# Kernel optimization log

Measured on AMD Instinct MI355X. Metric: run time of the kernel, lower is better.

Reference implementation:

```python
import jax, jax.numpy as jnp
import numpy as np

NUM_HEADS = 16
EMBED_DIM = 1024
HEAD_DIM = EMBED_DIM // NUM_HEADS


def _rel_shift(r):
    # r: (B, tlen, rlen). Pad with ONES (faithful to original), shift, tril.
    B, tlen, rlen = r.shape
    pad = jnp.ones((B, tlen, 1), dtype=r.dtype)
    rp = jnp.concatenate([pad, r], axis=2).reshape(B, rlen + 1, tlen)
    return jnp.tril(rp[:, 1:, :].reshape(B, tlen, rlen))


def setup_inputs() -> dict:
    key = jax.random.key(0)
    ks = jax.random.split(key, 12)
    T, B, E, H, D = 128, 8, EMBED_DIM, NUM_HEADS, HEAD_DIM
    query = jax.random.normal(ks[0], (T, B, E), dtype=jnp.float32)
    key_t = jax.random.normal(ks[1], (T, B, E), dtype=jnp.float32)
    value = jax.random.normal(ks[2], (T, B, E), dtype=jnp.float32)
    rel_pe = jax.random.normal(ks[3], (T, B, E), dtype=jnp.float32)
    # causal mask: True = masked (future positions)
    causal = ~jnp.tril(jnp.ones((T, T), dtype=bool))
    attn_mask = jnp.broadcast_to(causal, (B * H, T, T))
    utt_mask = jnp.ones((B * H, T, T, 1), dtype=jnp.float32)
    spk_mask = jax.random.randint(ks[4], (B, T, T), 0, 2, dtype=jnp.int32)
    s = 1.0 / np.sqrt(E)
    q_w = jax.random.uniform(ks[5], (E, E), jnp.float32, -s, s)
    k_w = jax.random.uniform(ks[6], (E, E), jnp.float32, -s, s)
    v_w = jax.random.uniform(ks[7], (E, E), jnp.float32, -s, s)
    r_w = jax.random.uniform(ks[8], (E, E), jnp.float32, -s, s)
    spk_emb = jax.random.uniform(ks[9], (2, E), jnp.float32, -s, s)
    out_w = jax.random.uniform(ks[10], (E, E), jnp.float32, -s, s)
    return {"query": query, "key": key_t, "value": value, "rel_pe": rel_pe,
            "attn_mask": attn_mask, "utt_mask": utt_mask, "spk_mask": spk_mask,
            "q_w": q_w, "k_w": k_w, "v_w": v_w, "r_w": r_w,
            "spk_emb": spk_emb, "out_w": out_w}


def reference(query, key, value, rel_pe, attn_mask, utt_mask, spk_mask,
              q_w, k_w, v_w, r_w, spk_emb, out_w):
    T, B, E = query.shape
    H, D = NUM_HEADS, HEAD_DIM
    scaling = float(D) ** -0.5

    def split_heads(x):  # (T, B, E) -> (B*H, T, D)
        return x.reshape(T, B * H, D).transpose(1, 0, 2)

    # NOTE: original computes k and v from `query` (faithful)
    q = split_heads(query @ q_w.T)
    k = split_heads(query @ k_w.T)
    v = split_heads(query @ v_w.T)
    r = split_heads(rel_pe @ r_w.T)

    # s_q: speaker embedding row 0 broadcast to all positions
    s_q = split_heads(jnp.broadcast_to(spk_emb[0], (T, B, E)))
    # s_k: (B, T, T, E) -> (B*H, T, T, D), same reshape chain as original
    s_k = spk_emb[spk_mask]                                   # (B, T, T, E)
    s_k = s_k.reshape(B, T * T, E).transpose(1, 0, 2)         # (T*T, B, E)
    s_k = s_k.reshape(T * T, B * H, D).transpose(1, 0, 2)     # (B*H, T*T, D)
    s_k = s_k.reshape(B * H, T, T, D) * utt_mask              # (B*H, T, T, D)

    new_q = q + s_q
    a1 = jnp.einsum('nid,njd->nij', new_q, k)
    a2 = jnp.einsum('nid,nijd->nij', new_q, s_k)
    a3 = _rel_shift(jnp.einsum('nid,njd->nij', s_q, r))

    w = (a1 + a2 + a3) * scaling
    w = jnp.where(attn_mask, jnp.asarray(1e-30, w.dtype), w)
    w = jax.nn.softmax(w, axis=-1)

    out = jnp.einsum('nij,njd->nid', w, v)                    # (B*H, T, D)
    out = out.transpose(1, 0, 2).reshape(T, B, E) @ out_w.T
    return out
```

## Files before the change

### kernel.cpp

```cpp
#include <hip/hip_runtime.h>
#include <hip/hip_bf16.h>
#include <cstddef>
#include <cstdint>


typedef _Float16 f16;
typedef __attribute__((ext_vector_type(8))) _Float16 f16x8;
typedef __attribute__((ext_vector_type(4))) float f32x4;

#define GLOBAL_TO_LDS(g, l) __builtin_amdgcn_global_load_lds( \
    (const __attribute__((address_space(1))) void*)(g),       \
    (__attribute__((address_space(3))) void*)(l), 16, 0, 0)

#define PIPE_SYNC(N) do {                                      \
    asm volatile("s_waitcnt vmcnt(" #N ")" ::: "memory");      \
    __builtin_amdgcn_s_barrier();                              \
    __builtin_amdgcn_sched_barrier(0);                         \
} while (0)

struct Ptr7 { const float* s[7]; };

__global__ __launch_bounds__(256) void tof16_kernel(Ptr7 p, f16* dbase)
{
    const float* s = p.s[blockIdx.y];
    f16* d = dbase + (size_t)blockIdx.y * (1u << 20);
    const int i = (blockIdx.x * 256 + threadIdx.x) * 8;
    const float4 a = *(const float4*)(s + i);
    const float4 b = *(const float4*)(s + i + 4);
    f16x8 o;
    o[0] = (f16)a.x; o[1] = (f16)a.y; o[2] = (f16)a.z; o[3] = (f16)a.w;
    o[4] = (f16)b.x; o[5] = (f16)b.y; o[6] = (f16)b.z; o[7] = (f16)b.w;
    *(f16x8*)(d + i) = o;
}

template <int TM, int TN, class Epi>
__device__ __forceinline__ void gemm3ph(const f16* __restrict__ A,
                                        const f16* __restrict__ B,
                                        int m0, int n0, Epi epi)
{
    constexpr int AITS = TM / 32, BITS = TN / 32;
    constexpr int LD = AITS + BITS;
    constexpr int FM = TM / 32, FN = TN / 32;
    __shared__ __attribute__((aligned(16))) f16 As0[TM * 64];
    __shared__ __attribute__((aligned(16))) f16 As1[TM * 64];
    __shared__ __attribute__((aligned(16))) f16 As2[TM * 64];
    __shared__ __attribute__((aligned(16))) f16 Bs0[TN * 64];
    __shared__ __attribute__((aligned(16))) f16 Bs1[TN * 64];
    __shared__ __attribute__((aligned(16))) f16 Bs2[TN * 64];
    const int tid = threadIdx.x;
    const int wave = tid >> 6, lane = tid & 63;
    const int wr = wave >> 1, wc = wave & 1;
    const int l16 = lane & 15, lk = lane >> 4;
    f32x4 acc[FM][FN] = {};

    auto stage = [&](f16* as_, f16* bs_, int k0) {
#pragma unroll
        for (int it = 0; it < AITS; ++it) {
            const int ebase = it * 2048 + wave * 512;
            const int e = ebase + lane * 8;
            const int row = e >> 6, slot = (e >> 3) & 7;
            const int scol = (slot ^ (row & 7)) << 3;
            GLOBAL_TO_LDS(A + (size_t)(m0 + row) * 1024 + k0 + scol, as_ + ebase);
        }
#pragma unroll
        for (int it = 0; it < BITS; ++it) {
            const int ebase = it * 2048 + wave * 512;
            const int e = ebase + lane * 8;
            const int row = e >> 6, slot = (e >> 3) & 7;
            const int scol = (slot ^ (row & 7)) << 3;
            GLOBAL_TO_LDS(B + (size_t)(n0 + row) * 1024 + k0 + scol, bs_ + ebase);
        }
    };
    auto compute = [&](const f16* as_, const f16* bs_) {
#pragma unroll
        for (int ksl = 0; ksl < 2; ++ksl) {
            const int s = ksl * 4 + lk;
            f16x8 af[FM], bg[FN];
#pragma unroll
            for (int mi = 0; mi < FM; ++mi) {
                const int r = wr * (TM / 2) + mi * 16 + l16;
                af[mi] = *(const f16x8*)(as_ + r * 64 + ((s ^ (r & 7)) << 3));
            }
#pragma unroll
            for (int ni = 0; ni < FN; ++ni) {
                const int r = wc * (TN / 2) + ni * 16 + l16;
                bg[ni] = *(const f16x8*)(bs_ + r * 64 + ((s ^ (r & 7)) << 3));
            }
#pragma unroll
            for (int mi = 0; mi < FM; ++mi)
#pragma unroll
                for (int ni = 0; ni < FN; ++ni)
                    acc[mi][ni] = __builtin_amdgcn_mfma_f32_16x16x32_f16(
                        af[mi], bg[ni], acc[mi][ni], 0, 0, 0);
        }
    };
    auto sync_steady = [&]() {
        if constexpr (LD == 8) PIPE_SYNC(8);
        else if constexpr (LD == 6) PIPE_SYNC(6);
        else PIPE_SYNC(5);
    };

    stage(As0, Bs0, 0);
    stage(As1, Bs1, 64);
    int k = 0;
#pragma unroll 1
    for (int t = 0; t < 15; t += 3) {
        sync_steady();
        if (t + 2 < 16) stage(As2, Bs2, k + 128);
        compute(As0, Bs0);
        sync_steady();
        if (t + 3 < 16) stage(As0, Bs0, k + 192);
        compute(As1, Bs1);
        sync_steady();
        if (t + 4 < 16) stage(As1, Bs1, k + 256);
        compute(As2, Bs2);
        k += 192;
    }
    PIPE_SYNC(0);
    compute(As0, Bs0);

#pragma unroll
    for (int mi = 0; mi < FM; ++mi)
#pragma unroll
        for (int ni = 0; ni < FN; ++ni)
#pragma unroll
            for (int r = 0; r < 4; ++r)
                epi(m0 + wr * (TM / 2) + mi * 16 + lk * 4 + r,
                    n0 + wc * (TN / 2) + ni * 16 + l16, acc[mi][ni][r]);
}

struct EpiHead {
    f16* dst; const float* addvec;
    __device__ void operator()(int row, int col, float v) const {
        const float x = addvec ? v + addvec[col] : v;
        const int b = row & 7, t = row >> 3, h = col >> 6, d = col & 63;
        dst[(size_t)(((b << 4) + h) * 128 + t) * 64 + d] = (f16)x;
    }
};
struct EpiF32 {
    float* dst;
    __device__ void operator()(int row, int col, float v) const {
        dst[(size_t)row * 1024 + col] = v;
    }
};

__global__ __launch_bounds__(256) void proj4_kernel(
    const f16* __restrict__ qf, const f16* __restrict__ rf,
    const f16* __restrict__ wbase, const float* __restrict__ spk_emb,
    f16* __restrict__ Qh, f16* __restrict__ Kh,
    f16* __restrict__ Vh, f16* __restrict__ Rh)
{
    const int bid = blockIdx.x;
    const int z = (bid & 7) >> 1;
    const int w = ((bid >> 3) << 1) | (bid & 1);
    const int m0 = (w >> 3) << 7;
    const int n0 = (w & 7) << 7;
    const f16* A = (z == 3) ? rf : qf;
    const f16* W = wbase + ((size_t)z << 20);
    f16* dst = (z == 0) ? Qh : (z == 1) ? Kh : (z == 2) ? Vh : Rh;
    EpiHead epi{dst, (z == 0) ? spk_emb : nullptr};
    gemm3ph<128, 128>(A, W, m0, n0, epi);
}

__global__ __launch_bounds__(256) void out_kernel(
    const f16* __restrict__ ATT, const f16* __restrict__ owf,
    float* __restrict__ out)
{
    const int bid = blockIdx.x;
    const int m0 = (bid >> 3) << 5;
    const int n0 = (bid & 7) << 7;
    EpiF32 epi{out};
    gemm3ph<32, 128>(ATT, owf, m0, n0, epi);
}

__global__ __launch_bounds__(256) void attn_mfma_kernel(
    const f16* __restrict__ Qh, const f16* __restrict__ Kh,
    const f16* __restrict__ Vh, const f16* __restrict__ Rh,
    const float* __restrict__ spk_emb, const int* __restrict__ spk_mask,
    const float* __restrict__ utt_mask, f16* __restrict__ ATT)
{
    __shared__ __attribute__((aligned(16))) char smem[58880];
    f16* nq = (f16*)smem;
    f16* kt = (f16*)(smem + 8192);
    f16* vt = (f16*)(smem + 24576);
    f16* vs = (f16*)(smem + 40960);
    float* cbuf = (float*)(smem + 57344);
    float* dd   = (float*)(smem + 57856);
    float* sq   = (float*)(smem + 58368);

    const int bx = blockIdx.x, n = bx >> 1, half = bx & 1;
    const int b = n >> 4, h = n & 15, i0 = half << 6;
    const int tid = threadIdx.x, wave = tid >> 6, lane = tid & 63;
    const int l16 = lane & 15, lk = lane >> 4;
    const int il0 = wave * 16 + lk * 4;
    const size_t hb = (size_t)n * (128 * 64);

    if (tid < 128)
        sq[tid] = spk_emb[(tid >> 6) * 1024 + (h << 6) + (tid & 63)];

#pragma unroll
    for (int it = 0; it < 2; ++it) {
        const int ebase = it * 2048 + wave * 512;
        const int e = ebase + lane * 8;
        const int row = e >> 6, slot = (e >> 3) & 7;
        const int scol = (slot ^ (row & 7)) << 3;
        GLOBAL_TO_LDS(Qh + hb + (size_t)(i0 + row) * 64 + scol, nq + ebase);
    }
#pragma unroll
    for (int it = 0; it < 4; ++it) {
        const int ebase = it * 2048 + wave * 512;
        const int e = ebase + lane * 8;
        const int row = e >> 6, slot = (e >> 3) & 7;
        const int scol = (slot ^ (row & 7)) << 3;
        GLOBAL_TO_LDS(Kh + hb + (size_t)row * 64 + scol, kt + ebase);
        GLOBAL_TO_LDS(Vh + hb + (size_t)row * 64 + scol, vs + ebase);
    }

    float du[8][4];
    int   sm[8][4];
#pragma unroll
    for (int ni = 0; ni < 8; ++ni) {
        const int j = ni * 16 + l16;
#pragma unroll
        for (int r = 0; r < 4; ++r) {
            const int i = i0 + il0 + r;
            du[ni][r] = utt_mask[((size_t)n * 128 + i) * 128 + j];
            sm[ni][r] = spk_mask[((size_t)b * 128 + i) * 128 + j];
        }
    }
    __syncthreads();

    {
        const int st = tid >> 1, hf = tid & 1;
        const int jt = st & 15, dt = st >> 4;
        f16x8 v[8];
#pragma unroll
        for (int jj = 0; jj < 8; ++jj) {
            const int j = jt * 8 + jj;
            v[jj] = *(const f16x8*)(vs + j * 64 + ((dt ^ (j & 7)) << 3));
        }
#pragma unroll
        for (int dr = 0; dr < 4; ++dr) {
            f16x8 w;
            int d;
            if (hf == 0) {
                d = dt * 8 + dr;
#pragma unroll
                for (int jj = 0; jj < 8; ++jj) w[jj] = v[jj][dr];
            } else {
                d = dt * 8 + 4 + dr;
#pragma unroll
                for (int jj = 0; jj < 8; ++jj) w[jj] = v[jj][4 + dr];
            }
            *(f16x8*)(vt + d * 128 + ((jt ^ (d & 7)) << 3)) = w;
        }
    }

    if (tid < 128) {
        const int j = tid;
        float s = 0.f;
#pragma unroll
        for (int c = 0; c < 8; ++c) {
            const f16x8 rv = *(const f16x8*)(Rh + hb + (size_t)j * 64 + c * 8);
#pragma unroll
            for (int e = 0; e < 8; ++e)
                s = fmaf((float)rv[e], sq[c * 8 + e], s);
        }
        cbuf[j] = s;
    } else if (tid < 192) {
        const int i = tid - 128;
        float s0 = 0.f, s1 = 0.f;
#pragma unroll
        for (int c = 0; c < 8; ++c) {
            const f16x8 qv = *(const f16x8*)(nq + i * 64 + ((c ^ (i & 7)) << 3));
#pragma unroll
            for (int e = 0; e < 8; ++e) {
                const float q = (float)qv[e];
                s0 = fmaf(q, sq[c * 8 + e], s0);
                s1 = fmaf(q, sq[64 + c * 8 + e], s1);
            }
        }
        dd[i] = s0; dd[64 + i] = s1;
    }
    __syncthreads();

    const int iw = wave * 16 + l16;
    f16x8 af[2];
#pragma unroll
    for (int ksl = 0; ksl < 2; ++ksl) {
        const int s = ksl * 4 + lk;
        af[ksl] = *(const f16x8*)(nq + iw * 64 + ((s ^ (iw & 7)) << 3));
    }
    f32x4 sacc[8] = {};
#pragma unroll
    for (int ksl = 0; ksl < 2; ++ksl) {
        const int s = ksl * 4 + lk;
#pragma unroll
        for (int ni = 0; ni < 8; ++ni) {
            const int j = ni * 16 + l16;
            const f16x8 bg = *(const f16x8*)(kt + j * 64 + ((s ^ (j & 7)) << 3));
            sacc[ni] = __builtin_amdgcn_mfma_f32_16x16x32_f16(af[ksl], bg, sacc[ni], 0, 0, 0);
        }
    }

    float sc[8][4];
#pragma unroll
    for (int ni = 0; ni < 8; ++ni) {
        const int j = ni * 16 + l16;
#pragma unroll
        for (int r = 0; r < 4; ++r) {
            const int il = il0 + r, i = i0 + il;
            const float a2 = du[ni][r] * (sm[ni][r] ? dd[64 + il] : dd[il]);
            const float a3 = (j <= i) ? cbuf[127 - i + j] : 0.f;
            const float v = (sacc[ni][r] + a2 + a3) * 0.125f;
            sc[ni][r] = (j > i) ? 1e-30f : v;
        }
    }
    float inv[4];
    f16* ps = vs + wave * 2048;
#pragma unroll
    for (int r = 0; r < 4; ++r) {
        float m = sc[0][r];
#pragma unroll
        for (int ni = 1; ni < 8; ++ni) m = fmaxf(m, sc[ni][r]);
#pragma unroll
        for (int off = 8; off > 0; off >>= 1) m = fmaxf(m, __shfl_xor(m, off, 64));
        float ssum = 0.f;
#pragma unroll
        for (int ni = 0; ni < 8; ++ni) {
            const float e = __expf(sc[ni][r] - m);
            sc[ni][r] = e;
            ssum += e;
        }
#pragma unroll
        for (int off = 8; off > 0; off >>= 1) ssum += __shfl_xor(ssum, off, 64);
        inv[r] = 1.f / ssum;
    }
#pragma unroll
    for (int ni = 0; ni < 8; ++ni) {
        const int j = ni * 16 + l16;
#pragma unroll
        for (int r = 0; r < 4; ++r) {
            const int il = lk * 4 + r;
            ps[il * 128 + ((((j >> 3) ^ (il & 7)) << 3) | (j & 7))] = (f16)sc[ni][r];
        }
    }

    f16x8 pa[4];
#pragma unroll
    for (int ks = 0; ks < 4; ++ks) {
        const int slot = ks * 4 + lk;
        pa[ks] = *(const f16x8*)(ps + l16 * 128 + ((slot ^ (l16 & 7)) << 3));
    }
    f32x4 oacc[4] = {};
#pragma unroll
    for (int ks = 0; ks < 4; ++ks) {
        const int slot = ks * 4 + lk;
#pragma unroll
        for (int nd = 0; nd < 4; ++nd) {
            const int d = nd * 16 + l16;
            const f16x8 vb = *(const f16x8*)(vt + d * 128 + ((slot ^ (d & 7)) << 3));
            oacc[nd] = __builtin_amdgcn_mfma_f32_16x16x32_f16(pa[ks], vb, oacc[nd], 0, 0, 0);
        }
    }
#pragma unroll
    for (int nd = 0; nd < 4; ++nd)
#pragma unroll
        for (int r = 0; r < 4; ++r) {
            const int i = i0 + il0 + r;
            const int col = (h << 6) + nd * 16 + l16;
            ATT[(size_t)(i * 8 + b) * 1024 + col] = (f16)(oacc[nd][r] * inv[r]);
        }
}

extern "C" void kernel_launch(void* const* d_in, const int* in_sizes, int n_in,
                              void* d_out, int out_size, void* d_ws, size_t ws_size,
                              hipStream_t stream)
{
    (void)in_sizes; (void)n_in; (void)out_size; (void)ws_size;

    const float* query  = (const float*)d_in[0];
    const float* rel_pe = (const float*)d_in[3];
    const float* utt    = (const float*)d_in[5];
    const int*   spk    = (const int*)d_in[6];
    const float* qw     = (const float*)d_in[7];
    const float* kw     = (const float*)d_in[8];
    const float* vw     = (const float*)d_in[9];
    const float* rw     = (const float*)d_in[10];
    const float* spke   = (const float*)d_in[11];
    const float* ow     = (const float*)d_in[12];

    char* ws = (char*)d_ws;
    f16* Qh  = (f16*)(ws);
    f16* Kh  = (f16*)(ws + (2u  << 20));
    f16* Vh  = (f16*)(ws + (4u  << 20));
    f16* Rh  = (f16*)(ws + (6u  << 20));
    f16* ATT = (f16*)(ws + (8u  << 20));
    f16* fb  = (f16*)(ws + (10u << 20));

    f16* qf = fb;
    f16* rf = fb + (1u << 20);
    f16* wb = fb + (2u << 20);
    f16* ob = fb + (6u << 20);

    Ptr7 p7;
    p7.s[0] = query; p7.s[1] = rel_pe; p7.s[2] = qw; p7.s[3] = kw;
    p7.s[4] = vw; p7.s[5] = rw; p7.s[6] = ow;

    tof16_kernel<<<dim3(512, 7), 256, 0, stream>>>(p7, fb);
    proj4_kernel<<<dim3(256), 256, 0, stream>>>(qf, rf, wb, spke, Qh, Kh, Vh, Rh);
    attn_mfma_kernel<<<dim3(256), 256, 0, stream>>>(Qh, Kh, Vh, Rh, spke, spk, utt, ATT);
    out_kernel<<<dim3(256), 256, 0, stream>>>(ATT, ob, (float*)d_out);
}
```

Measured before the change: 51.85 us.

## Fuse speaker/rel dot-products into projection epilogue and write V transposed

The projection GEMM epilogue now computes the q·spk and r·spk_emb[0] reductions directly and stores them as small float vectors (DD, CB), and writes V pre-transposed. This replaces the full R projection store and removes the in-attention V transpose and dot-product passes, along with a barrier. The projection tile is halved to 64x128 with twice the blocks for better occupancy across CUs. In exchange the epilogue gains cross-lane shuffle reductions and strided transposed V stores that coalesce poorly.

```diff
diff --git a/kernel.cpp b/kernel.cpp
--- a/kernel.cpp
+++ b/kernel.cpp
@@ -33,10 +33,11 @@
     *(f16x8*)(d + i) = o;
 }
 
-template <int TM, int TN, class Epi>
-__device__ __forceinline__ void gemm3ph(const f16* __restrict__ A,
-                                        const f16* __restrict__ B,
-                                        int m0, int n0, Epi epi)
+template <int TM, int TN>
+__device__ __forceinline__ void gemm3ph_acc(const f16* __restrict__ A,
+                                            const f16* __restrict__ B,
+                                            int m0, int n0,
+                                            f32x4 (&acc)[TM / 32][TN / 32])
 {
     constexpr int AITS = TM / 32, BITS = TN / 32;
     constexpr int LD = AITS + BITS;
@@ -51,7 +52,6 @@
     const int wave = tid >> 6, lane = tid & 63;
     const int wr = wave >> 1, wc = wave & 1;
     const int l16 = lane & 15, lk = lane >> 4;
-    f32x4 acc[FM][FN] = {};
 
     auto stage = [&](f16* as_, f16* bs_, int k0) {
 #pragma unroll
@@ -95,9 +95,7 @@
         }
     };
     auto sync_steady = [&]() {
-        if constexpr (LD == 8) PIPE_SYNC(8);
-        else if constexpr (LD == 6) PIPE_SYNC(6);
-        else PIPE_SYNC(5);
+        if constexpr (LD == 6) PIPE_SYNC(6); else PIPE_SYNC(5);
     };
 
     stage(As0, Bs0, 0);
@@ -118,48 +116,105 @@
     }
     PIPE_SYNC(0);
     compute(As0, Bs0);
-
-#pragma unroll
-    for (int mi = 0; mi < FM; ++mi)
-#pragma unroll
-        for (int ni = 0; ni < FN; ++ni)
-#pragma unroll
-            for (int r = 0; r < 4; ++r)
-                epi(m0 + wr * (TM / 2) + mi * 16 + lk * 4 + r,
-                    n0 + wc * (TN / 2) + ni * 16 + l16, acc[mi][ni][r]);
-}
-
-struct EpiHead {
-    f16* dst; const float* addvec;
-    __device__ void operator()(int row, int col, float v) const {
-        const float x = addvec ? v + addvec[col] : v;
-        const int b = row & 7, t = row >> 3, h = col >> 6, d = col & 63;
-        dst[(size_t)(((b << 4) + h) * 128 + t) * 64 + d] = (f16)x;
-    }
-};
-struct EpiF32 {
-    float* dst;
-    __device__ void operator()(int row, int col, float v) const {
-        dst[(size_t)row * 1024 + col] = v;
-    }
-};
+}
 
 __global__ __launch_bounds__(256) void proj4_kernel(
     const f16* __restrict__ qf, const f16* __restrict__ rf,
     const f16* __restrict__ wbase, const float* __restrict__ spk_emb,
-    f16* __restrict__ Qh, f16* __restrict__ Kh,
-    f16* __restrict__ Vh, f16* __restrict__ Rh)
+    f16* __restrict__ Qh, f16* __restrict__ Kh, f16* __restrict__ VhT,
+    float* __restrict__ CB, float* __restrict__ DD)
 {
     const int bid = blockIdx.x;
     const int z = (bid & 7) >> 1;
     const int w = ((bid >> 3) << 1) | (bid & 1);
-    const int m0 = (w >> 3) << 7;
+    const int m0 = (w >> 3) << 6;
     const int n0 = (w & 7) << 7;
     const f16* A = (z == 3) ? rf : qf;
     const f16* W = wbase + ((size_t)z << 20);
-    f16* dst = (z == 0) ? Qh : (z == 1) ? Kh : (z == 2) ? Vh : Rh;
-    EpiHead epi{dst, (z == 0) ? spk_emb : nullptr};
-    gemm3ph<128, 128>(A, W, m0, n0, epi);
+
+    f32x4 acc[2][4] = {};
+    gemm3ph_acc<64, 128>(A, W, m0, n0, acc);
+
+    const int tid = threadIdx.x;
+    const int wave = tid >> 6, lane = tid & 63;
+    const int wr = wave >> 1, wc = wave & 1;
+    const int l16 = lane & 15, lk = lane >> 4;
+    const int h = (n0 >> 6) + wc;
+
+    if (z == 0) {
+        float s0v[4], s1v[4];
+#pragma unroll
+        for (int ni = 0; ni < 4; ++ni) {
+            const int c = (h << 6) + ni * 16 + l16;
+            s0v[ni] = spk_emb[c];
+            s1v[ni] = spk_emb[1024 + c];
+        }
+#pragma unroll
+        for (int mi = 0; mi < 2; ++mi)
+#pragma unroll
+            for (int r = 0; r < 4; ++r) {
+                const int row = m0 + wr * 32 + mi * 16 + lk * 4 + r;
+                const int b = row & 7, t = row >> 3;
+                float p0 = 0.f, p1 = 0.f;
+#pragma unroll
+                for (int ni = 0; ni < 4; ++ni) {
+                    const float x = acc[mi][ni][r] + s0v[ni];
+                    const int d = ni * 16 + l16;
+                    Qh[(size_t)(((b << 4) + h) * 128 + t) * 64 + d] = (f16)x;
+                    p0 = fmaf(x, s0v[ni], p0);
+                    p1 = fmaf(x, s1v[ni], p1);
+                }
+#pragma unroll
+                for (int off = 1; off < 16; off <<= 1) {
+                    p0 += __shfl_xor(p0, off, 64);
+                    p1 += __shfl_xor(p1, off, 64);
+                }
+                if (l16 == 0) {
+                    const int n = (b << 4) + h;
+                    DD[n * 128 + t] = p0;
+                    DD[16384 + n * 128 + t] = p1;
+                }
+            }
+    } else if (z == 3) {
+        float s0v[4];
+#pragma unroll
+        for (int ni = 0; ni < 4; ++ni)
+            s0v[ni] = spk_emb[(h << 6) + ni * 16 + l16];
+#pragma unroll
+        for (int mi = 0; mi < 2; ++mi)
+#pragma unroll
+            for (int r = 0; r < 4; ++r) {
+                const int row = m0 + wr * 32 + mi * 16 + lk * 4 + r;
+                const int b = row & 7, j = row >> 3;
+                float p = 0.f;
+#pragma unroll
+                for (int ni = 0; ni < 4; ++ni)
+                    p = fmaf(acc[mi][ni][r], s0v[ni], p);
+#pragma unroll
+                for (int off = 1; off < 16; off <<= 1)
+                    p += __shfl_xor(p, off, 64);
+                if (l16 == 0)
+                    CB[((b << 4) + h) * 128 + j] = p;
+            }
+    } else {
+        f16* dst = (z == 1) ? Kh : VhT;
+#pragma unroll
+        for (int mi = 0; mi < 2; ++mi)
+#pragma unroll
+            for (int r = 0; r < 4; ++r) {
+                const int row = m0 + wr * 32 + mi * 16 + lk * 4 + r;
+                const int b = row & 7, t = row >> 3;
+#pragma unroll
+                for (int ni = 0; ni < 4; ++ni) {
+                    const int d = ni * 16 + l16;
+                    const f16 x = (f16)acc[mi][ni][r];
+                    if (z == 1)
+                        dst[(size_t)(((b << 4) + h) * 128 + t) * 64 + d] = x;
+                    else
+                        dst[(size_t)(((b << 4) + h) * 64 + d) * 128 + t] = x;
+                }
+            }
+    }
 }
 
 __global__ __launch_bounds__(256) void out_kernel(
@@ -169,24 +224,36 @@
     const int bid = blockIdx.x;
     const int m0 = (bid >> 3) << 5;
     const int n0 = (bid & 7) << 7;
-    EpiF32 epi{out};
-    gemm3ph<32, 128>(ATT, owf, m0, n0, epi);
+    f32x4 acc[1][4] = {};
+    gemm3ph_acc<32, 128>(ATT, owf, m0, n0, acc);
+    const int tid = threadIdx.x;
+    const int wave = tid >> 6, lane = tid & 63;
+    const int wr = wave >> 1, wc = wave & 1;
+    const int l16 = lane & 15, lk = lane >> 4;
+#pragma unroll
+    for (int ni = 0; ni < 4; ++ni)
+#pragma unroll
+        for (int r = 0; r < 4; ++r) {
+            const int row = m0 + wr * 16 + lk * 4 + r;
+            const int col = n0 + wc * 64 + ni * 16 + l16;
+            out[(size_t)row * 1024 + col] = acc[0][ni][r];
+        }
 }
 
 __global__ __launch_bounds__(256) void attn_mfma_kernel(
     const f16* __restrict__ Qh, const f16* __restrict__ Kh,
-    const f16* __restrict__ Vh, const f16* __restrict__ Rh,
-    const float* __restrict__ spk_emb, const int* __restrict__ spk_mask,
-    const float* __restrict__ utt_mask, f16* __restrict__ ATT)
-{
-    __shared__ __attribute__((aligned(16))) char smem[58880];
+    const f16* __restrict__ VhT,
+    const float* __restrict__ CB, const float* __restrict__ DD,
+    const int* __restrict__ spk_mask, const float* __restrict__ utt_mask,
+    f16* __restrict__ ATT)
+{
+    __shared__ __attribute__((aligned(16))) char smem[58368];
     f16* nq = (f16*)smem;
     f16* kt = (f16*)(smem + 8192);
     f16* vt = (f16*)(smem + 24576);
-    f16* vs = (f16*)(smem + 40960);
+    f16* psb = (f16*)(smem + 40960);
     float* cbuf = (float*)(smem + 57344);
-    float* dd   = (float*)(smem + 57856);
-    float* sq   = (float*)(smem + 58368);
+    float* ddl  = (float*)(smem + 57856);
 
     const int bx = blockIdx.x, n = bx >> 1, half = bx & 1;
     const int b = n >> 4, h = n & 15, i0 = half << 6;
@@ -195,9 +262,6 @@
     const int il0 = wave * 16 + lk * 4;
     const size_t hb = (size_t)n * (128 * 64);
 
-    if (tid < 128)
-        sq[tid] = spk_emb[(tid >> 6) * 1024 + (h << 6) + (tid & 63)];
-
 #pragma unroll
     for (int it = 0; it < 2; ++it) {
         const int ebase = it * 2048 + wave * 512;
@@ -213,7 +277,21 @@
         const int row = e >> 6, slot = (e >> 3) & 7;
         const int scol = (slot ^ (row & 7)) << 3;
         GLOBAL_TO_LDS(Kh + hb + (size_t)row * 64 + scol, kt + ebase);
-        GLOBAL_TO_LDS(Vh + hb + (size_t)row * 64 + scol, vs + ebase);
+    }
+#pragma unroll
+    for (int it = 0; it < 4; ++it) {
+        const int ebase = it * 2048 + wave * 512;
+        const int e = ebase + lane * 8;
+        const int row = e >> 7, slot = (e >> 3) & 15;
+        const int scol = (slot ^ (row & 7)) << 3;
+        GLOBAL_TO_LDS(VhT + hb + (size_t)row * 128 + scol, vt + ebase);
+    }
+
+    if (tid < 128) {
+        cbuf[tid] = CB[n * 128 + tid];
+    } else {
+        const int t2 = tid - 128;
+        ddl[t2] = DD[(t2 >> 6) * 16384 + n * 128 + i0 + (t2 & 63)];
     }
 
     float du[8][4];
@@ -230,60 +308,6 @@
     }
     __syncthreads();
 
-    {
-        const int st = tid >> 1, hf = tid & 1;
-        const int jt = st & 15, dt = st >> 4;
-        f16x8 v[8];
-#pragma unroll
-        for (int jj = 0; jj < 8; ++jj) {
-            const int j = jt * 8 + jj;
-            v[jj] = *(const f16x8*)(vs + j * 64 + ((dt ^ (j & 7)) << 3));
-        }
-#pragma unroll
-        for (int dr = 0; dr < 4; ++dr) {
-            f16x8 w;
-            int d;
-            if (hf == 0) {
-                d = dt * 8 + dr;
-#pragma unroll
-                for (int jj = 0; jj < 8; ++jj) w[jj] = v[jj][dr];
-            } else {
-                d = dt * 8 + 4 + dr;
-#pragma unroll
-                for (int jj = 0; jj < 8; ++jj) w[jj] = v[jj][4 + dr];
-            }
-            *(f16x8*)(vt + d * 128 + ((jt ^ (d & 7)) << 3)) = w;
-        }
-    }
-
-    if (tid < 128) {
-        const int j = tid;
-        float s = 0.f;
-#pragma unroll
-        for (int c = 0; c < 8; ++c) {
-            const f16x8 rv = *(const f16x8*)(Rh + hb + (size_t)j * 64 + c * 8);
-#pragma unroll
-            for (int e = 0; e < 8; ++e)
-                s = fmaf((float)rv[e], sq[c * 8 + e], s);
-        }
-        cbuf[j] = s;
-    } else if (tid < 192) {
-        const int i = tid - 128;
-        float s0 = 0.f, s1 = 0.f;
-#pragma unroll
-        for (int c = 0; c < 8; ++c) {
-            const f16x8 qv = *(const f16x8*)(nq + i * 64 + ((c ^ (i & 7)) << 3));
-#pragma unroll
-            for (int e = 0; e < 8; ++e) {
-                const float q = (float)qv[e];
-                s0 = fmaf(q, sq[c * 8 + e], s0);
-                s1 = fmaf(q, sq[64 + c * 8 + e], s1);
-            }
-        }
-        dd[i] = s0; dd[64 + i] = s1;
-    }
-    __syncthreads();
-
     const int iw = wave * 16 + l16;
     f16x8 af[2];
 #pragma unroll
@@ -310,14 +334,14 @@
 #pragma unroll
         for (int r = 0; r < 4; ++r) {
             const int il = il0 + r, i = i0 + il;
-            const float a2 = du[ni][r] * (sm[ni][r] ? dd[64 + il] : dd[il]);
+            const float a2 = du[ni][r] * (sm[ni][r] ? ddl[64 + il] : ddl[il]);
             const float a3 = (j <= i) ? cbuf[127 - i + j] : 0.f;
             const float v = (sacc[ni][r] + a2 + a3) * 0.125f;
             sc[ni][r] = (j > i) ? 1e-30f : v;
         }
     }
     float inv[4];
-    f16* ps = vs + wave * 2048;
+    f16* ps = psb + wave * 2048;
 #pragma unroll
     for (int r = 0; r < 4; ++r) {
         float m = sc[0][r];
@@ -391,12 +415,13 @@
     const float* ow     = (const float*)d_in[12];
 
     char* ws = (char*)d_ws;
-    f16* Qh  = (f16*)(ws);
-    f16* Kh  = (f16*)(ws + (2u  << 20));
-    f16* Vh  = (f16*)(ws + (4u  << 20));
-    f16* Rh  = (f16*)(ws + (6u  << 20));
-    f16* ATT = (f16*)(ws + (8u  << 20));
-    f16* fb  = (f16*)(ws + (10u << 20));
+    f16* Qh   = (f16*)(ws);
+    f16* Kh   = (f16*)(ws + (2u  << 20));
+    f16* VhT  = (f16*)(ws + (4u  << 20));
+    f16* ATT  = (f16*)(ws + (6u  << 20));
+    float* CB = (float*)(ws + (8u  << 20));
+    float* DD = (float*)(ws + (8u << 20) + (256u << 10));
+    f16* fb   = (f16*)(ws + (10u << 20));
 
     f16* qf = fb;
     f16* rf = fb + (1u << 20);
@@ -408,7 +433,7 @@
     p7.s[4] = vw; p7.s[5] = rw; p7.s[6] = ow;
 
     tof16_kernel<<<dim3(512, 7), 256, 0, stream>>>(p7, fb);
-    proj4_kernel<<<dim3(256), 256, 0, stream>>>(qf, rf, wb, spke, Qh, Kh, Vh, Rh);
-    attn_mfma_kernel<<<dim3(256), 256, 0, stream>>>(Qh, Kh, Vh, Rh, spke, spk, utt, ATT);
+    proj4_kernel<<<dim3(512), 256, 0, stream>>>(qf, rf, wb, spke, Qh, Kh, VhT, CB, DD);
+    attn_mfma_kernel<<<dim3(256), 256, 0, stream>>>(Qh, Kh, VhT, CB, DD, spk, utt, ATT);
     out_kernel<<<dim3(256), 256, 0, stream>>>(ATT, ob, (float*)d_out);
 }
```

New measurement: 49.28 us. -4.9%, faster.
